# Kernel optimization log

Hardware: AMD Instinct MI355X
Metric: run time of the kernel (lower is better)

Reference implementation:

```python
import jax, jax.numpy as jnp
import numpy as np

B, T, NG = 1024, 16, 23            # clips, window, nodes per timestep graph
H, IN, L, C = 64, 8, 20, 3         # hidden, input_dim, num_layers, classes
E_PER = 256                        # edges per graph
NUM_GRAPHS = B * T                 # 16384
N = NUM_GRAPHS * NG                # 376832 nodes
E = NUM_GRAPHS * E_PER             # 4194304 edges
LN_EPS = 1e-5


def setup_inputs() -> dict:
    key = jax.random.key(0)
    ks = jax.random.split(key, 16)
    s = 0.05
    x = jax.random.normal(ks[0], (N, IN), jnp.float32)
    # intra-graph random edges: global_id = graph_id * NG + local_id
    gid = jnp.repeat(jnp.arange(NUM_GRAPHS, dtype=jnp.int32), E_PER)
    src_l = jax.random.randint(ks[1], (E,), 0, NG, dtype=jnp.int32)
    dst_l = jax.random.randint(ks[2], (E,), 0, NG, dtype=jnp.int32)
    edge_index = jnp.stack([gid * NG + src_l, gid * NG + dst_l])
    batch = jnp.repeat(jnp.arange(NUM_GRAPHS, dtype=jnp.int32), NG)
    return {
        "x": x,
        "edge_index": edge_index,
        "batch": batch,
        "W_enc": jax.random.normal(ks[3], (IN, H), jnp.float32) * s,
        "b_enc": jnp.zeros((H,), jnp.float32),
        "ln_g": jnp.ones((L, H), jnp.float32),
        "ln_b": jnp.zeros((L, H), jnp.float32),
        "W_rel": jax.random.normal(ks[4], (L, H, H), jnp.float32) * s,
        "b_rel": jnp.zeros((L, H), jnp.float32),
        "W_root": jax.random.normal(ks[5], (L, H, H), jnp.float32) * s,
        "pos": jax.random.normal(ks[6], (1, T, H), jnp.float32) * 0.02,
        "W1": jax.random.normal(ks[7], (H, H), jnp.float32) * s,
        "b1": jnp.zeros((H,), jnp.float32),
        "W2": jax.random.normal(ks[8], (H, C), jnp.float32) * s,
        "b2": jnp.zeros((C,), jnp.float32),
    }


def _layer_norm(h, g, b):
    mu = jnp.mean(h, axis=-1, keepdims=True)
    var = jnp.mean(jnp.square(h - mu), axis=-1, keepdims=True)
    return (h - mu) * jax.lax.rsqrt(var + LN_EPS) * g + b


def reference(x, edge_index, batch, W_enc, b_enc, ln_g, ln_b, W_rel, b_rel,
              W_root, pos, W1, b1, W2, b2):
    src, dst = edge_index[0], edge_index[1]
    h = x @ W_enc + b_enc                      # node encoder, [N, H]

    # DeepGCNLayer block='res+': out = x + GraphConv(relu(LN(x)))
    # GraphConv: lin_rel(sum_{j->i} z_j) + lin_root(z)  (aggr='add')
    def step(h, p):
        g, b, Wr, br, Wo = p
        z = jax.nn.relu(_layer_norm(h, g, b))  # dropout = identity (eval)
        agg = jax.ops.segment_sum(z[src], dst, num_segments=N)
        return h + agg @ Wr + br + z @ Wo, None

    h, _ = jax.lax.scan(step, h, (ln_g, ln_b, W_rel, b_rel, W_root))

    # global mean pool (each graph has exactly NG nodes)
    pooled = jax.ops.segment_sum(h, batch, num_segments=NUM_GRAPHS) / NG
    xt = pooled.reshape(B, T, H) + pos[:, :T, :]
    v = jnp.mean(xt, axis=1)                   # temporal 'pool'
    h1 = jax.nn.relu(v @ W1 + b1)
    return h1 @ W2 + b2                        # [B, C]
```

## Files before the change

kernel.cpp:

```cpp
#include <hip/hip_runtime.h>
#include <hip/hip_bf16.h>

#define NGRAPH 16384
#define NPAIR  (NGRAPH / 2)
#define NG     23
#define PCOLS  46
#define HD     64
#define INF    8
#define LAYERS 20
#define EDGES_PER 256
#define E_TOT  (NGRAPH * EDGES_PER)
#define BATCH  1024
#define TWIN   16
#define CLS    3

#define NS 64

typedef __attribute__((ext_vector_type(8))) short s8v;
typedef __attribute__((ext_vector_type(4))) float f4v;
typedef __attribute__((ext_vector_type(2))) float f2v;

union FragU { unsigned u[4]; s8v v; };

__device__ inline f2v vlo(f4v v) { return (f2v){v[0], v[1]}; }
__device__ inline f2v vhi(f4v v) { return (f2v){v[2], v[3]}; }

__device__ inline unsigned pk2_bf16(f2v v) {
  __hip_bfloat162 b = __float22bfloat162_rn(make_float2(v[0], v[1]));
  unsigned r;
  __builtin_memcpy(&r, &b, sizeof(r));
  return r;
}

__device__ inline f2v max0(f2v v) {
#if defined(__has_builtin) && __has_builtin(__builtin_elementwise_max)
  return __builtin_elementwise_max(v, (f2v){0.f, 0.f});
#else
  return (f2v){fmaxf(v[0], 0.f), fmaxf(v[1], 0.f)};
#endif
}

__device__ inline unsigned f2bf_pk(float a, float b) {
  unsigned ua = __builtin_bit_cast(unsigned, a);
  unsigned ub = __builtin_bit_cast(unsigned, b);
  ua = ua + 0x7FFFu + ((ua >> 16) & 1u);
  ub = ub + 0x7FFFu + ((ub >> 16) & 1u);
  return (ua >> 16) | (ub & 0xFFFF0000u);
}

__global__ __launch_bounds__(256) void pack_w(const float* __restrict__ W_rel,
                                              const float* __restrict__ W_root,
                                              unsigned* __restrict__ wf) {
  const int tid = blockIdx.x * 256 + threadIdx.x;
  if (tid >= LAYERS * 2 * 4 * 2 * 64) return;
  const int lane = tid & 63, fi = tid >> 6;
  const int Kt = fi & 1, Mt = (fi >> 1) & 3, m = (fi >> 3) & 1, l = fi >> 4;
  const float* W = (m ? W_root : W_rel) + (size_t)l * HD * HD;
  const int col = lane & 15, quad = lane >> 4;
  const int jdim = Mt * 16 + col;
  unsigned pk[4];
#pragma unroll
  for (int w = 0; w < 4; ++w) {
    const int j0 = 2 * w, j1 = 2 * w + 1;
    const int d0 = ((j0 >> 2) * 2 + Kt) * 16 + quad * 4 + (j0 & 3);
    const int d1 = ((j1 >> 2) * 2 + Kt) * 16 + quad * 4 + (j1 & 3);
    pk[w] = f2bf_pk(W[(size_t)d0 * HD + jdim], W[(size_t)d1 * HD + jdim]);
  }
  uint4 q; q.x = pk[0]; q.y = pk[1]; q.z = pk[2]; q.w = pk[3];
  *(uint4*)&wf[(size_t)tid * 4] = q;
}

__global__ __launch_bounds__(256) void build_padj(const int* __restrict__ ei,
                                                  unsigned* __restrict__ adjf) {
  __shared__ unsigned cnt[4][48 * 24];
  const int lane = threadIdx.x & 63, wv = threadIdx.x >> 6;
  const int p = blockIdx.x * 4 + wv;
  const int col = lane & 15, quad = lane >> 4;
  unsigned* c = cnt[wv];
  for (int i = lane; i < 48 * 24; i += 64) c[i] = 0;
  asm volatile("s_waitcnt lgkmcnt(0)" ::: "memory");
  const int ebase = p * (2 * EDGES_PER);
  const int noff = p * PCOLS;
#pragma unroll
  for (int r = 0; r < 8; ++r) {
    const int e = ebase + r * 64 + lane;
    const int s = ei[e] - noff;
    const int d = ei[E_TOT + e] - noff;
    atomicAdd(&c[d * 24 + (s >> 1)], 1u << ((s & 1) * 16));
  }
  asm volatile("s_waitcnt lgkmcnt(0)" ::: "memory");
#pragma unroll
  for (int Nt = 0; Nt < 3; ++Nt) {
    const int dst = col + 16 * Nt;
    const bool dok = dst < PCOLS;
#pragma unroll
    for (int Kt = 0; Kt < 2; ++Kt) {
      unsigned pk[4];
#pragma unroll
      for (int w = 0; w < 4; ++w) {
        const int s0 = Kt * 32 + quad * 8 + 2 * w;
        float v0 = 0.f, v1 = 0.f;
        if (dok && s0 < PCOLS) {
          const unsigned rd = c[dst * 24 + (s0 >> 1)];
          v0 = (float)(rd & 0xffffu);
          if (s0 + 1 < PCOLS) v1 = (float)(rd >> 16);
        }
        pk[w] = f2bf_pk(v0, v1);
      }
      uint4 q; q.x = pk[0]; q.y = pk[1]; q.z = pk[2]; q.w = pk[3];
      ((uint4*)adjf)[((size_t)p * 6 + Nt * 2 + Kt) * 64 + lane] = q;
    }
  }
}

__global__ __launch_bounds__(256, 4) void gcn_main(
    const float* __restrict__ x, const unsigned* __restrict__ adjf,
    const unsigned* __restrict__ wf,
    const float* __restrict__ W_enc, const float* __restrict__ b_enc,
    const float* __restrict__ ln_g, const float* __restrict__ ln_b,
    const float* __restrict__ b_rel, float* __restrict__ pooled) {
  __shared__ __align__(16) unsigned short sm[4 * HD * NS];
  const int lane = threadIdx.x & 63, wv = threadIdx.x >> 6;
  const int p = blockIdx.x * 4 + wv;
  const int col = lane & 15, quad = lane >> 4;
  unsigned short* zt = sm + wv * (HD * NS);

  {
    uint4 z4; z4.x = 0; z4.y = 0; z4.z = 0; z4.w = 0;
    for (int i = lane; i < (HD * NS * 2) / 16; i += 64) ((uint4*)zt)[i] = z4;
  }
  asm volatile("s_waitcnt lgkmcnt(0)" ::: "memory");

  const uint4* ap  = (const uint4*)adjf + (size_t)p * 384 + lane;
  const uint4* ap4 = ap + 256;

  const int c7 = (col >> 1) & 7;
  const int ra0 = col * NS + ((quad ^ c7) << 3);
  const unsigned short* zA = zt + ra0;
  const unsigned short* zB = zt + (ra0 ^ 32);
  int wb[3][2];
#pragma unroll
  for (int Nt = 0; Nt < 3; ++Nt) {
    const int node = col + 16 * Nt;
    wb[Nt][0] = (quad * 4    ) * NS + (((node >> 3) ^ (quad * 2    )) << 3) + (node & 7);
    wb[Nt][1] = (quad * 4 + 2) * NS + (((node >> 3) ^ (quad * 2 + 1)) << 3) + (node & 7);
  }

  f4v acc[4][3];
  {
    const float* xg = x + (size_t)p * PCOLS * INF;
    f4v xa[3][2];
    const f4v zz = {0.f, 0.f, 0.f, 0.f};
#pragma unroll
    for (int Nt = 0; Nt < 3; ++Nt) {
      const int c = col + 16 * Nt;
      if (c < PCOLS) {
        const float* xp = xg + (size_t)c * INF;
        xa[Nt][0] = *(const f4v*)xp;
        xa[Nt][1] = *(const f4v*)(xp + 4);
      } else { xa[Nt][0] = zz; xa[Nt][1] = zz; }
    }
#pragma unroll
    for (int Mt = 0; Mt < 4; ++Mt) {
      const f4v be = *(const f4v*)(b_enc + Mt * 16 + quad * 4);
      acc[Mt][0] = be; acc[Mt][1] = be; acc[Mt][2] = be;
#pragma unroll
      for (int i = 0; i < INF; ++i) {
        const f4v we = *(const f4v*)(W_enc + i * HD + Mt * 16 + quad * 4);
        acc[Mt][0] += we * xa[0][i >> 2][i & 3];
        acc[Mt][1] += we * xa[1][i >> 2][i & 3];
        acc[Mt][2] += we * xa[2][i >> 2][i & 3];
      }
    }
  }

#pragma unroll 1
  for (int l = 0; l < LAYERS; ++l) {
    const unsigned* wbase = wf + (size_t)l * (2 * 4 * 2 * 64 * 4);

    float mu[3], rs[3];
    {
      float sh[3], qh[3];
#pragma unroll
      for (int Nt = 0; Nt < 3; ++Nt) {
        f2v t = vlo(acc[0][Nt]) + vhi(acc[0][Nt]);
        t += vlo(acc[1][Nt]); t += vhi(acc[1][Nt]);
        t += vlo(acc[2][Nt]); t += vhi(acc[2][Nt]);
        t += vlo(acc[3][Nt]); t += vhi(acc[3][Nt]);
        f2v u = vlo(acc[0][Nt]) * vlo(acc[0][Nt]);
        u += vhi(acc[0][Nt]) * vhi(acc[0][Nt]);
        u += vlo(acc[1][Nt]) * vlo(acc[1][Nt]);
        u += vhi(acc[1][Nt]) * vhi(acc[1][Nt]);
        u += vlo(acc[2][Nt]) * vlo(acc[2][Nt]);
        u += vhi(acc[2][Nt]) * vhi(acc[2][Nt]);
        u += vlo(acc[3][Nt]) * vlo(acc[3][Nt]);
        u += vhi(acc[3][Nt]) * vhi(acc[3][Nt]);
        sh[Nt] = t[0] + t[1];
        qh[Nt] = u[0] + u[1];
      }
#pragma unroll
      for (int Nt = 0; Nt < 3; ++Nt) { sh[Nt] += __shfl_xor(sh[Nt], 16); qh[Nt] += __shfl_xor(qh[Nt], 16); }
#pragma unroll
      for (int Nt = 0; Nt < 3; ++Nt) { sh[Nt] += __shfl_xor(sh[Nt], 32); qh[Nt] += __shfl_xor(qh[Nt], 32); }
#pragma unroll
      for (int Nt = 0; Nt < 3; ++Nt) {
        mu[Nt] = sh[Nt] * (1.0f / HD);
        float var = fmaf(qh[Nt], (1.0f / HD), -mu[Nt] * mu[Nt]);
        var = fmaxf(var, 0.f);
        rs[Nt] = rsqrtf(var + 1e-5f);
      }
    }

    FragU zpk[2][3];
#pragma unroll
    for (int Kt = 0; Kt < 2; ++Kt) {
#pragma unroll
      for (int hi = 0; hi < 2; ++hi) {
        const int Mt = Kt + 2 * hi;
        const f4v gf  = *(const f4v*)(ln_g + l * HD + Mt * 16 + quad * 4);
        const f4v bfv = *(const f4v*)(ln_b + l * HD + Mt * 16 + quad * 4);
        const f2v gl = vlo(gf), gh = vhi(gf);
        const f2v bl = vlo(bfv), bh = vhi(bfv);
#pragma unroll
        for (int Nt = 0; Nt < 3; ++Nt) {
          const f2v sgl = gl * rs[Nt], sgh = gh * rs[Nt];
          const f2v tbl = bl - mu[Nt] * sgl, tbh = bh - mu[Nt] * sgh;
          const f2v zl = max0(vlo(acc[Mt][Nt]) * sgl + tbl);
          const f2v zh = max0(vhi(acc[Mt][Nt]) * sgh + tbh);
          zpk[Kt][Nt].u[hi * 2 + 0] = pk2_bf16(zl);
          zpk[Kt][Nt].u[hi * 2 + 1] = pk2_bf16(zh);
        }
      }
#pragma unroll
      for (int hi = 0; hi < 2; ++hi) {
        const int Mt = Kt + 2 * hi;
#pragma unroll
        for (int Nt = 0; Nt < 3; ++Nt)
#pragma unroll
          for (int r2 = 0; r2 < 2; ++r2) {
            const unsigned d = zpk[Kt][Nt].u[hi * 2 + r2];
            unsigned short* pz = zt + Mt * 1024 + wb[Nt][r2];
            pz[0]  = (unsigned short)d;
            pz[NS] = (unsigned short)(d >> 16);
          }
      }
    }

#pragma unroll
    for (int Kt = 0; Kt < 2; ++Kt)
#pragma unroll
      for (int Mt = 0; Mt < 4; ++Mt) {
        const s8v wo = *(const s8v*)&wbase[((((1 * 4) + Mt) * 2 + Kt) * 64 + lane) * 4];
#pragma unroll
        for (int Nt = 0; Nt < 3; ++Nt)
          acc[Mt][Nt] = __builtin_amdgcn_mfma_f32_16x16x32_bf16(wo, zpk[Kt][Nt].v, acc[Mt][Nt], 0, 0, 0);
      }

    FragU adjB[3][2];
#pragma unroll
    for (int idx = 0; idx < 4; ++idx)
      adjB[idx >> 1][idx & 1].v = *(const s8v*)(ap + idx * 64);
    adjB[2][0].v = *(const s8v*)(ap4);
    adjB[2][1].v = *(const s8v*)(ap4 + 64);

    asm volatile("s_waitcnt lgkmcnt(0)" ::: "memory");

    const f4v zzero = {0.f, 0.f, 0.f, 0.f};
#pragma unroll
    for (int Kt = 0; Kt < 2; ++Kt) {
      const s8v zaA0 = *(const s8v*)&zA[(Kt    ) * 1024];
      const s8v zaA1 = *(const s8v*)&zB[(Kt    ) * 1024];
      const s8v zaC0 = *(const s8v*)&zA[(Kt + 2) * 1024];
      const s8v zaC1 = *(const s8v*)&zB[(Kt + 2) * 1024];
      FragU apk[3];
#pragma unroll
      for (int Nt = 0; Nt < 3; ++Nt) {
        f4v agA = __builtin_amdgcn_mfma_f32_16x16x32_bf16(zaA0, adjB[Nt][0].v, zzero, 0, 0, 0);
        agA     = __builtin_amdgcn_mfma_f32_16x16x32_bf16(zaA1, adjB[Nt][1].v, agA,   0, 0, 0);
        f4v agC = __builtin_amdgcn_mfma_f32_16x16x32_bf16(zaC0, adjB[Nt][0].v, zzero, 0, 0, 0);
        agC     = __builtin_amdgcn_mfma_f32_16x16x32_bf16(zaC1, adjB[Nt][1].v, agC,   0, 0, 0);
        apk[Nt].u[0] = pk2_bf16(vlo(agA));
        apk[Nt].u[1] = pk2_bf16(vhi(agA));
        apk[Nt].u[2] = pk2_bf16(vlo(agC));
        apk[Nt].u[3] = pk2_bf16(vhi(agC));
      }
#pragma unroll
      for (int Mt = 0; Mt < 4; ++Mt) {
        const s8v wr = *(const s8v*)&wbase[((((0 * 4) + Mt) * 2 + Kt) * 64 + lane) * 4];
#pragma unroll
        for (int Nt = 0; Nt < 3; ++Nt)
          acc[Mt][Nt] = __builtin_amdgcn_mfma_f32_16x16x32_bf16(wr, apk[Nt].v, acc[Mt][Nt], 0, 0, 0);
      }
    }

#pragma unroll
    for (int Mt = 0; Mt < 4; ++Mt) {
      const f4v brf = *(const f4v*)(b_rel + l * HD + Mt * 16 + quad * 4);
      const f2v bl = vlo(brf), bh = vhi(brf);
#pragma unroll
      for (int Nt = 0; Nt < 3; ++Nt) {
        const f2v al = vlo(acc[Mt][Nt]) + bl;
        const f2v ah = vhi(acc[Mt][Nt]) + bh;
        acc[Mt][Nt] = (f4v){al[0], al[1], ah[0], ah[1]};
      }
    }
  }

  float* hb = (float*)zt;
  asm volatile("s_waitcnt lgkmcnt(0)" ::: "memory");
#pragma unroll
  for (int Mt = 0; Mt < 4; ++Mt)
#pragma unroll
    for (int Nt = 0; Nt < 2; ++Nt)
      *(f4v*)&hb[(col + 16 * Nt) * HD + Mt * 16 + quad * 4] = acc[Mt][Nt];
  asm volatile("s_waitcnt lgkmcnt(0)" ::: "memory");
  float sA = 0.f, sB = 0.f;
#pragma unroll
  for (int c = 0; c < NG; ++c) sA += hb[c * HD + lane];
#pragma unroll
  for (int c = NG; c < 32; ++c) sB += hb[c * HD + lane];
  asm volatile("s_waitcnt lgkmcnt(0)" ::: "memory");
#pragma unroll
  for (int Mt = 0; Mt < 4; ++Mt)
    *(f4v*)&hb[col * HD + Mt * 16 + quad * 4] = acc[Mt][2];
  asm volatile("s_waitcnt lgkmcnt(0)" ::: "memory");
#pragma unroll
  for (int c = 0; c < PCOLS - 32; ++c) sB += hb[c * HD + lane];
  pooled[(size_t)(2 * p) * HD + lane] = sA;
  pooled[(size_t)(2 * p + 1) * HD + lane] = sB;
}

__global__ __launch_bounds__(64) void head(
    const float* __restrict__ pooled, const float* __restrict__ pos,
    const float* __restrict__ W1, const float* __restrict__ b1,
    const float* __restrict__ W2, const float* __restrict__ b2,
    float* __restrict__ out) {
  __shared__ float sv[HD];
  __shared__ float sh1[HD];
  const int b = blockIdx.x, k = threadIdx.x;
  float v = 0.f;
#pragma unroll
  for (int tt = 0; tt < TWIN; ++tt) v += pooled[((size_t)(b * TWIN + tt)) * HD + k];
  float p = 0.f;
#pragma unroll
  for (int tt = 0; tt < TWIN; ++tt) p += pos[tt * HD + k];
  v = v * (1.0f / (NG * TWIN)) + p * (1.0f / TWIN);
  sv[k] = v;
  __syncthreads();
  float a = b1[k];
#pragma unroll
  for (int kk = 0; kk < HD; ++kk) a = fmaf(sv[kk], W1[kk * HD + k], a);
  a = fmaxf(a, 0.f);
  sh1[k] = a;
  __syncthreads();
  if (k < CLS) {
    float o = b2[k];
#pragma unroll
    for (int kk = 0; kk < HD; ++kk) o = fmaf(sh1[kk], W2[kk * CLS + k], o);
    out[(size_t)b * CLS + k] = o;
  }
}

extern "C" void kernel_launch(void* const* d_in, const int* in_sizes, int n_in,
                              void* d_out, int out_size, void* d_ws, size_t ws_size,
                              hipStream_t stream) {
  const float* x      = (const float*)d_in[0];
  const int*   ei     = (const int*)  d_in[1];
  const float* W_enc  = (const float*)d_in[3];
  const float* b_enc  = (const float*)d_in[4];
  const float* ln_g   = (const float*)d_in[5];
  const float* ln_b   = (const float*)d_in[6];
  const float* W_rel  = (const float*)d_in[7];
  const float* b_rel  = (const float*)d_in[8];
  const float* W_root = (const float*)d_in[9];
  const float* pos    = (const float*)d_in[10];
  const float* W1     = (const float*)d_in[11];
  const float* b1     = (const float*)d_in[12];
  const float* W2     = (const float*)d_in[13];
  const float* b2     = (const float*)d_in[14];
  float* out = (float*)d_out;

  char* pp = (char*)d_ws;
  unsigned* wfrag   = (unsigned*)pp;  pp += (size_t)LAYERS * 2 * 4 * 2 * 64 * 16;
  unsigned* adjfrag = (unsigned*)pp;  pp += (size_t)NPAIR * 6 * 64 * 16;
  float*    pooled  = (float*)pp;

  pack_w    <<<80, 256, 0, stream>>>(W_rel, W_root, wfrag);
  build_padj<<<NPAIR / 4, 256, 0, stream>>>(ei, adjfrag);
  gcn_main  <<<NPAIR / 4, 256, 0, stream>>>(x, adjfrag, wfrag, W_enc, b_enc,
                                            ln_g, ln_b, b_rel, pooled);
  head      <<<BATCH, 64, 0, stream>>>(pooled, pos, W1, b1, W2, b2, out);
}
```

Before: 429.0 us.

## Process two graph pairs per wavefront to reuse weight fragments

Each wavefront now handles two graph pairs instead of one, with blocks shrunk to 128 threads so each block still covers four pairs. Per-layer weight, LayerNorm parameter and bias loads are shared across both pairs, and interleaving two independent MFMA chains gives more instruction-level parallelism. In exchange the accumulator state doubles per wave, which raises register pressure and reduces occupancy (launch bounds go to 128 threads with min 2 blocks).

```diff
diff --git a/kernel.cpp b/kernel.cpp
--- a/kernel.cpp
+++ b/kernel.cpp
@@ -113,31 +113,34 @@
   }
 }
 
-__global__ __launch_bounds__(256, 4) void gcn_main(
+__global__ __launch_bounds__(128, 2) void gcn_main(
     const float* __restrict__ x, const unsigned* __restrict__ adjf,
     const unsigned* __restrict__ wf,
     const float* __restrict__ W_enc, const float* __restrict__ b_enc,
     const float* __restrict__ ln_g, const float* __restrict__ ln_b,
     const float* __restrict__ b_rel, float* __restrict__ pooled) {
-  __shared__ __align__(16) unsigned short sm[4 * HD * NS];
+  __shared__ __align__(16) unsigned short sm[2 * 2 * HD * NS];
   const int lane = threadIdx.x & 63, wv = threadIdx.x >> 6;
-  const int p = blockIdx.x * 4 + wv;
+  const int pbase = blockIdx.x * 4 + wv * 2;
   const int col = lane & 15, quad = lane >> 4;
-  unsigned short* zt = sm + wv * (HD * NS);
+  unsigned short* zt[2] = { sm + (wv * 2 + 0) * (HD * NS),
+                            sm + (wv * 2 + 1) * (HD * NS) };
 
   {
     uint4 z4; z4.x = 0; z4.y = 0; z4.z = 0; z4.w = 0;
-    for (int i = lane; i < (HD * NS * 2) / 16; i += 64) ((uint4*)zt)[i] = z4;
+    uint4* d = (uint4*)(sm + (size_t)wv * 2 * (HD * NS));
+    for (int i = lane; i < (2 * HD * NS * 2) / 16; i += 64) d[i] = z4;
   }
   asm volatile("s_waitcnt lgkmcnt(0)" ::: "memory");
 
-  const uint4* ap  = (const uint4*)adjf + (size_t)p * 384 + lane;
-  const uint4* ap4 = ap + 256;
+  const uint4* ap[2];
+#pragma unroll
+  for (int q = 0; q < 2; ++q)
+    ap[q] = (const uint4*)adjf + (size_t)(pbase + q) * 384 + lane;
 
   const int c7 = (col >> 1) & 7;
   const int ra0 = col * NS + ((quad ^ c7) << 3);
-  const unsigned short* zA = zt + ra0;
-  const unsigned short* zB = zt + (ra0 ^ 32);
+  const int ra1 = ra0 ^ 32;
   int wb[3][2];
 #pragma unroll
   for (int Nt = 0; Nt < 3; ++Nt) {
@@ -146,9 +149,10 @@
     wb[Nt][1] = (quad * 4 + 2) * NS + (((node >> 3) ^ (quad * 2 + 1)) << 3) + (node & 7);
   }
 
-  f4v acc[4][3];
-  {
-    const float* xg = x + (size_t)p * PCOLS * INF;
+  f4v acc[2][4][3];
+#pragma unroll
+  for (int q = 0; q < 2; ++q) {
+    const float* xg = x + (size_t)(pbase + q) * PCOLS * INF;
     f4v xa[3][2];
     const f4v zz = {0.f, 0.f, 0.f, 0.f};
 #pragma unroll
@@ -163,13 +167,13 @@
 #pragma unroll
     for (int Mt = 0; Mt < 4; ++Mt) {
       const f4v be = *(const f4v*)(b_enc + Mt * 16 + quad * 4);
-      acc[Mt][0] = be; acc[Mt][1] = be; acc[Mt][2] = be;
+      acc[q][Mt][0] = be; acc[q][Mt][1] = be; acc[q][Mt][2] = be;
 #pragma unroll
       for (int i = 0; i < INF; ++i) {
         const f4v we = *(const f4v*)(W_enc + i * HD + Mt * 16 + quad * 4);
-        acc[Mt][0] += we * xa[0][i >> 2][i & 3];
-        acc[Mt][1] += we * xa[1][i >> 2][i & 3];
-        acc[Mt][2] += we * xa[2][i >> 2][i & 3];
+        acc[q][Mt][0] += we * xa[0][i >> 2][i & 3];
+        acc[q][Mt][1] += we * xa[1][i >> 2][i & 3];
+        acc[q][Mt][2] += we * xa[2][i >> 2][i & 3];
       }
     }
   }
@@ -178,23 +182,24 @@
   for (int l = 0; l < LAYERS; ++l) {
     const unsigned* wbase = wf + (size_t)l * (2 * 4 * 2 * 64 * 4);
 
-    float mu[3], rs[3];
-    {
+    float mu[2][3], rs[2][3];
+#pragma unroll
+    for (int q = 0; q < 2; ++q) {
       float sh[3], qh[3];
 #pragma unroll
       for (int Nt = 0; Nt < 3; ++Nt) {
-        f2v t = vlo(acc[0][Nt]) + vhi(acc[0][Nt]);
-        t += vlo(acc[1][Nt]); t += vhi(acc[1][Nt]);
-        t += vlo(acc[2][Nt]); t += vhi(acc[2][Nt]);
-        t += vlo(acc[3][Nt]); t += vhi(acc[3][Nt]);
-        f2v u = vlo(acc[0][Nt]) * vlo(acc[0][Nt]);
-        u += vhi(acc[0][Nt]) * vhi(acc[0][Nt]);
-        u += vlo(acc[1][Nt]) * vlo(acc[1][Nt]);
-        u += vhi(acc[1][Nt]) * vhi(acc[1][Nt]);
-        u += vlo(acc[2][Nt]) * vlo(acc[2][Nt]);
-        u += vhi(acc[2][Nt]) * vhi(acc[2][Nt]);
-        u += vlo(acc[3][Nt]) * vlo(acc[3][Nt]);
-        u += vhi(acc[3][Nt]) * vhi(acc[3][Nt]);
+        f2v t = vlo(acc[q][0][Nt]) + vhi(acc[q][0][Nt]);
+        t += vlo(acc[q][1][Nt]); t += vhi(acc[q][1][Nt]);
+        t += vlo(acc[q][2][Nt]); t += vhi(acc[q][2][Nt]);
+        t += vlo(acc[q][3][Nt]); t += vhi(acc[q][3][Nt]);
+        f2v u = vlo(acc[q][0][Nt]) * vlo(acc[q][0][Nt]);
+        u += vhi(acc[q][0][Nt]) * vhi(acc[q][0][Nt]);
+        u += vlo(acc[q][1][Nt]) * vlo(acc[q][1][Nt]);
+        u += vhi(acc[q][1][Nt]) * vhi(acc[q][1][Nt]);
+        u += vlo(acc[q][2][Nt]) * vlo(acc[q][2][Nt]);
+        u += vhi(acc[q][2][Nt]) * vhi(acc[q][2][Nt]);
+        u += vlo(acc[q][3][Nt]) * vlo(acc[q][3][Nt]);
+        u += vhi(acc[q][3][Nt]) * vhi(acc[q][3][Nt]);
         sh[Nt] = t[0] + t[1];
         qh[Nt] = u[0] + u[1];
       }
@@ -204,92 +209,102 @@
       for (int Nt = 0; Nt < 3; ++Nt) { sh[Nt] += __shfl_xor(sh[Nt], 32); qh[Nt] += __shfl_xor(qh[Nt], 32); }
 #pragma unroll
       for (int Nt = 0; Nt < 3; ++Nt) {
-        mu[Nt] = sh[Nt] * (1.0f / HD);
-        float var = fmaf(qh[Nt], (1.0f / HD), -mu[Nt] * mu[Nt]);
+        mu[q][Nt] = sh[Nt] * (1.0f / HD);
+        float var = fmaf(qh[Nt], (1.0f / HD), -mu[q][Nt] * mu[q][Nt]);
         var = fmaxf(var, 0.f);
-        rs[Nt] = rsqrtf(var + 1e-5f);
-      }
-    }
-
-    FragU zpk[2][3];
-#pragma unroll
-    for (int Kt = 0; Kt < 2; ++Kt) {
-#pragma unroll
-      for (int hi = 0; hi < 2; ++hi) {
-        const int Mt = Kt + 2 * hi;
-        const f4v gf  = *(const f4v*)(ln_g + l * HD + Mt * 16 + quad * 4);
-        const f4v bfv = *(const f4v*)(ln_b + l * HD + Mt * 16 + quad * 4);
-        const f2v gl = vlo(gf), gh = vhi(gf);
-        const f2v bl = vlo(bfv), bh = vhi(bfv);
+        rs[q][Nt] = rsqrtf(var + 1e-5f);
+      }
+    }
+
+#pragma unroll
+    for (int q = 0; q < 2; ++q) {
+      FragU zpk[2][3];
+#pragma unroll
+      for (int Kt = 0; Kt < 2; ++Kt) {
+#pragma unroll
+        for (int hi = 0; hi < 2; ++hi) {
+          const int Mt = Kt + 2 * hi;
+          const f4v gf  = *(const f4v*)(ln_g + l * HD + Mt * 16 + quad * 4);
+          const f4v bfv = *(const f4v*)(ln_b + l * HD + Mt * 16 + quad * 4);
+          const f2v gl = vlo(gf), gh = vhi(gf);
+          const f2v bl = vlo(bfv), bh = vhi(bfv);
+#pragma unroll
+          for (int Nt = 0; Nt < 3; ++Nt) {
+            const f2v sgl = gl * rs[q][Nt], sgh = gh * rs[q][Nt];
+            const f2v tbl = bl - mu[q][Nt] * sgl, tbh = bh - mu[q][Nt] * sgh;
+            const f2v zl = max0(vlo(acc[q][Mt][Nt]) * sgl + tbl);
+            const f2v zh = max0(vhi(acc[q][Mt][Nt]) * sgh + tbh);
+            zpk[Kt][Nt].u[hi * 2 + 0] = pk2_bf16(zl);
+            zpk[Kt][Nt].u[hi * 2 + 1] = pk2_bf16(zh);
+          }
+        }
+#pragma unroll
+        for (int hi = 0; hi < 2; ++hi) {
+          const int Mt = Kt + 2 * hi;
+#pragma unroll
+          for (int Nt = 0; Nt < 3; ++Nt)
+#pragma unroll
+            for (int r2 = 0; r2 < 2; ++r2) {
+              const unsigned d = zpk[Kt][Nt].u[hi * 2 + r2];
+              unsigned short* pz = zt[q] + Mt * 1024 + wb[Nt][r2];
+              pz[0]  = (unsigned short)d;
+              pz[NS] = (unsigned short)(d >> 16);
+            }
+        }
+      }
+#pragma unroll
+      for (int Kt = 0; Kt < 2; ++Kt)
+#pragma unroll
+        for (int Mt = 0; Mt < 4; ++Mt) {
+          const s8v wo = *(const s8v*)&wbase[((((1 * 4) + Mt) * 2 + Kt) * 64 + lane) * 4];
+#pragma unroll
+          for (int Nt = 0; Nt < 3; ++Nt)
+            acc[q][Mt][Nt] = __builtin_amdgcn_mfma_f32_16x16x32_bf16(wo, zpk[Kt][Nt].v, acc[q][Mt][Nt], 0, 0, 0);
+        }
+    }
+
+    FragU adjB[2][3][2];
+#pragma unroll
+    for (int q = 0; q < 2; ++q) {
+#pragma unroll
+      for (int idx = 0; idx < 4; ++idx)
+        adjB[q][idx >> 1][idx & 1].v = *(const s8v*)(ap[q] + idx * 64);
+      adjB[q][2][0].v = *(const s8v*)(ap[q] + 256);
+      adjB[q][2][1].v = *(const s8v*)(ap[q] + 320);
+    }
+
+    asm volatile("s_waitcnt lgkmcnt(0)" ::: "memory");
+
+    const f4v zzero = {0.f, 0.f, 0.f, 0.f};
+#pragma unroll
+    for (int q = 0; q < 2; ++q) {
+      const unsigned short* zAq = zt[q] + ra0;
+      const unsigned short* zBq = zt[q] + ra1;
+#pragma unroll
+      for (int Kt = 0; Kt < 2; ++Kt) {
+        const s8v zaA0 = *(const s8v*)&zAq[(Kt    ) * 1024];
+        const s8v zaA1 = *(const s8v*)&zBq[(Kt    ) * 1024];
+        const s8v zaC0 = *(const s8v*)&zAq[(Kt + 2) * 1024];
+        const s8v zaC1 = *(const s8v*)&zBq[(Kt + 2) * 1024];
+        FragU apk[3];
 #pragma unroll
         for (int Nt = 0; Nt < 3; ++Nt) {
-          const f2v sgl = gl * rs[Nt], sgh = gh * rs[Nt];
-          const f2v tbl = bl - mu[Nt] * sgl, tbh = bh - mu[Nt] * sgh;
-          const f2v zl = max0(vlo(acc[Mt][Nt]) * sgl + tbl);
-          const f2v zh = max0(vhi(acc[Mt][Nt]) * sgh + tbh);
-          zpk[Kt][Nt].u[hi * 2 + 0] = pk2_bf16(zl);
-          zpk[Kt][Nt].u[hi * 2 + 1] = pk2_bf16(zh);
-        }
-      }
-#pragma unroll
-      for (int hi = 0; hi < 2; ++hi) {
-        const int Mt = Kt + 2 * hi;
-#pragma unroll
-        for (int Nt = 0; Nt < 3; ++Nt)
-#pragma unroll
-          for (int r2 = 0; r2 < 2; ++r2) {
-            const unsigned d = zpk[Kt][Nt].u[hi * 2 + r2];
-            unsigned short* pz = zt + Mt * 1024 + wb[Nt][r2];
-            pz[0]  = (unsigned short)d;
-            pz[NS] = (unsigned short)(d >> 16);
-          }
-      }
-    }
-
-#pragma unroll
-    for (int Kt = 0; Kt < 2; ++Kt)
-#pragma unroll
-      for (int Mt = 0; Mt < 4; ++Mt) {
-        const s8v wo = *(const s8v*)&wbase[((((1 * 4) + Mt) * 2 + Kt) * 64 + lane) * 4];
-#pragma unroll
-        for (int Nt = 0; Nt < 3; ++Nt)
-          acc[Mt][Nt] = __builtin_amdgcn_mfma_f32_16x16x32_bf16(wo, zpk[Kt][Nt].v, acc[Mt][Nt], 0, 0, 0);
-      }
-
-    FragU adjB[3][2];
-#pragma unroll
-    for (int idx = 0; idx < 4; ++idx)
-      adjB[idx >> 1][idx & 1].v = *(const s8v*)(ap + idx * 64);
-    adjB[2][0].v = *(const s8v*)(ap4);
-    adjB[2][1].v = *(const s8v*)(ap4 + 64);
-
-    asm volatile("s_waitcnt lgkmcnt(0)" ::: "memory");
-
-    const f4v zzero = {0.f, 0.f, 0.f, 0.f};
-#pragma unroll
-    for (int Kt = 0; Kt < 2; ++Kt) {
-      const s8v zaA0 = *(const s8v*)&zA[(Kt    ) * 1024];
-      const s8v zaA1 = *(const s8v*)&zB[(Kt    ) * 1024];
-      const s8v zaC0 = *(const s8v*)&zA[(Kt + 2) * 1024];
-      const s8v zaC1 = *(const s8v*)&zB[(Kt + 2) * 1024];
-      FragU apk[3];
-#pragma unroll
-      for (int Nt = 0; Nt < 3; ++Nt) {
-        f4v agA = __builtin_amdgcn_mfma_f32_16x16x32_bf16(zaA0, adjB[Nt][0].v, zzero, 0, 0, 0);
-        agA     = __builtin_amdgcn_mfma_f32_16x16x32_bf16(zaA1, adjB[Nt][1].v, agA,   0, 0, 0);
-        f4v agC = __builtin_amdgcn_mfma_f32_16x16x32_bf16(zaC0, adjB[Nt][0].v, zzero, 0, 0, 0);
-        agC     = __builtin_amdgcn_mfma_f32_16x16x32_bf16(zaC1, adjB[Nt][1].v, agC,   0, 0, 0);
-        apk[Nt].u[0] = pk2_bf16(vlo(agA));
-        apk[Nt].u[1] = pk2_bf16(vhi(agA));
-        apk[Nt].u[2] = pk2_bf16(vlo(agC));
-        apk[Nt].u[3] = pk2_bf16(vhi(agC));
-      }
-#pragma unroll
-      for (int Mt = 0; Mt < 4; ++Mt) {
-        const s8v wr = *(const s8v*)&wbase[((((0 * 4) + Mt) * 2 + Kt) * 64 + lane) * 4];
-#pragma unroll
-        for (int Nt = 0; Nt < 3; ++Nt)
-          acc[Mt][Nt] = __builtin_amdgcn_mfma_f32_16x16x32_bf16(wr, apk[Nt].v, acc[Mt][Nt], 0, 0, 0);
+          f4v agA = __builtin_amdgcn_mfma_f32_16x16x32_bf16(zaA0, adjB[q][Nt][0].v, zzero, 0, 0, 0);
+          agA     = __builtin_amdgcn_mfma_f32_16x16x32_bf16(zaA1, adjB[q][Nt][1].v, agA,   0, 0, 0);
+          f4v agC = __builtin_amdgcn_mfma_f32_16x16x32_bf16(zaC0, adjB[q][Nt][0].v, zzero, 0, 0, 0);
+          agC     = __builtin_amdgcn_mfma_f32_16x16x32_bf16(zaC1, adjB[q][Nt][1].v, agC,   0, 0, 0);
+          apk[Nt].u[0] = pk2_bf16(vlo(agA));
+          apk[Nt].u[1] = pk2_bf16(vhi(agA));
+          apk[Nt].u[2] = pk2_bf16(vlo(agC));
+          apk[Nt].u[3] = pk2_bf16(vhi(agC));
+        }
+#pragma unroll
+        for (int Mt = 0; Mt < 4; ++Mt) {
+          const s8v wr = *(const s8v*)&wbase[((((0 * 4) + Mt) * 2 + Kt) * 64 + lane) * 4];
+#pragma unroll
+          for (int Nt = 0; Nt < 3; ++Nt)
+            acc[q][Mt][Nt] = __builtin_amdgcn_mfma_f32_16x16x32_bf16(wr, apk[Nt].v, acc[q][Mt][Nt], 0, 0, 0);
+        }
       }
     }
 
@@ -298,36 +313,42 @@
       const f4v brf = *(const f4v*)(b_rel + l * HD + Mt * 16 + quad * 4);
       const f2v bl = vlo(brf), bh = vhi(brf);
 #pragma unroll
-      for (int Nt = 0; Nt < 3; ++Nt) {
-        const f2v al = vlo(acc[Mt][Nt]) + bl;
-        const f2v ah = vhi(acc[Mt][Nt]) + bh;
-        acc[Mt][Nt] = (f4v){al[0], al[1], ah[0], ah[1]};
-      }
-    }
-  }
-
-  float* hb = (float*)zt;
-  asm volatile("s_waitcnt lgkmcnt(0)" ::: "memory");
-#pragma unroll
-  for (int Mt = 0; Mt < 4; ++Mt)
-#pragma unroll
-    for (int Nt = 0; Nt < 2; ++Nt)
-      *(f4v*)&hb[(col + 16 * Nt) * HD + Mt * 16 + quad * 4] = acc[Mt][Nt];
-  asm volatile("s_waitcnt lgkmcnt(0)" ::: "memory");
-  float sA = 0.f, sB = 0.f;
-#pragma unroll
-  for (int c = 0; c < NG; ++c) sA += hb[c * HD + lane];
-#pragma unroll
-  for (int c = NG; c < 32; ++c) sB += hb[c * HD + lane];
-  asm volatile("s_waitcnt lgkmcnt(0)" ::: "memory");
-#pragma unroll
-  for (int Mt = 0; Mt < 4; ++Mt)
-    *(f4v*)&hb[col * HD + Mt * 16 + quad * 4] = acc[Mt][2];
-  asm volatile("s_waitcnt lgkmcnt(0)" ::: "memory");
-#pragma unroll
-  for (int c = 0; c < PCOLS - 32; ++c) sB += hb[c * HD + lane];
-  pooled[(size_t)(2 * p) * HD + lane] = sA;
-  pooled[(size_t)(2 * p + 1) * HD + lane] = sB;
+      for (int q = 0; q < 2; ++q)
+#pragma unroll
+        for (int Nt = 0; Nt < 3; ++Nt) {
+          const f2v al = vlo(acc[q][Mt][Nt]) + bl;
+          const f2v ah = vhi(acc[q][Mt][Nt]) + bh;
+          acc[q][Mt][Nt] = (f4v){al[0], al[1], ah[0], ah[1]};
+        }
+    }
+  }
+
+#pragma unroll
+  for (int q = 0; q < 2; ++q) {
+    float* hb = (float*)zt[q];
+    asm volatile("s_waitcnt lgkmcnt(0)" ::: "memory");
+#pragma unroll
+    for (int Mt = 0; Mt < 4; ++Mt)
+#pragma unroll
+      for (int Nt = 0; Nt < 2; ++Nt)
+        *(f4v*)&hb[(col + 16 * Nt) * HD + Mt * 16 + quad * 4] = acc[q][Mt][Nt];
+    asm volatile("s_waitcnt lgkmcnt(0)" ::: "memory");
+    float sA = 0.f, sB = 0.f;
+#pragma unroll
+    for (int c = 0; c < NG; ++c) sA += hb[c * HD + lane];
+#pragma unroll
+    for (int c = NG; c < 32; ++c) sB += hb[c * HD + lane];
+    asm volatile("s_waitcnt lgkmcnt(0)" ::: "memory");
+#pragma unroll
+    for (int Mt = 0; Mt < 4; ++Mt)
+      *(f4v*)&hb[col * HD + Mt * 16 + quad * 4] = acc[q][Mt][2];
+    asm volatile("s_waitcnt lgkmcnt(0)" ::: "memory");
+#pragma unroll
+    for (int c = 0; c < PCOLS - 32; ++c) sB += hb[c * HD + lane];
+    const int pq = pbase + q;
+    pooled[(size_t)(2 * pq) * HD + lane] = sA;
+    pooled[(size_t)(2 * pq + 1) * HD + lane] = sB;
+  }
 }
 
 __global__ __launch_bounds__(64) void head(
@@ -387,7 +408,7 @@
 
   pack_w    <<<80, 256, 0, stream>>>(W_rel, W_root, wfrag);
   build_padj<<<NPAIR / 4, 256, 0, stream>>>(ei, adjfrag);
-  gcn_main  <<<NPAIR / 4, 256, 0, stream>>>(x, adjfrag, wfrag, W_enc, b_enc,
+  gcn_main  <<<NPAIR / 4, 128, 0, stream>>>(x, adjfrag, wfrag, W_enc, b_enc,
                                             ln_g, ln_b, b_rel, pooled);
   head      <<<BATCH, 64, 0, stream>>>(pooled, pos, W1, b1, W2, b2, out);
 }
```

Result: slower. 513.4 us (+19.7%).
